# Performance work log

Measured on AMD Instinct MI355X. Metric: run time of the kernel, lower is better.

## Reference

```python
import jax, jax.numpy as jnp
import numpy as np

B, N1, N2, D = 4, 8192, 8192, 3

def setup_inputs() -> dict:
    key = jax.random.key(0)
    k1, k2 = jax.random.split(key)
    xyz1 = jax.random.normal(k1, (B, N1, D), dtype=jnp.float32)
    xyz2 = jax.random.normal(k2, (B, N2, D), dtype=jnp.float32)
    return {"xyz1": xyz1, "xyz2": xyz2}

def reference(xyz1, xyz2):
    # Pairwise squared distances via ||a-b||^2 = ||a||^2 + ||b||^2 - 2 a.b
    sq1 = jnp.sum(xyz1 * xyz1, axis=-1)                     # [B, N1]
    sq2 = jnp.sum(xyz2 * xyz2, axis=-1)                     # [B, N2]
    cross = jnp.einsum("bnd,bmd->bnm", xyz1, xyz2)          # [B, N1, N2]
    d = sq1[:, :, None] + sq2[:, None, :] - 2.0 * cross     # [B, N1, N2]
    dist1 = jnp.min(d, axis=2)                              # nearest in xyz2 for each xyz1 point
    dist2 = jnp.min(d, axis=1)                              # nearest in xyz1 for each xyz2 point
    return jnp.mean(dist1) + jnp.mean(dist2)                # reduction='mean'
```

## Files before the change

kernel.cpp:

```cpp
#include <hip/hip_runtime.h>
#include <math.h>

#define BATCH 4
#define NPTS  8192
#define TOTAL (BATCH * NPTS)
#define TPB   256

#define CT     2
#define WPB    (TPB / 64)
#define COLS_PER_WAVE  (32 * CT)
#define COLS_PER_BLOCK (COLS_PER_WAVE * WPB)
#define ROWCH  16
#define SWEEP  (NPTS / ROWCH)
#define NT     (SWEEP / 32)

typedef __bf16 bf16v8 __attribute__((ext_vector_type(8)));
typedef float  f32x16 __attribute__((ext_vector_type(16)));


__device__ __forceinline__ unsigned f2ord(float f) {
  unsigned b = __float_as_uint(f);
  return ((int)b >= 0) ? (b ^ 0x80000000u) : ~b;
}
__device__ __forceinline__ float ord2f(unsigned k) {
  unsigned b = (k & 0x80000000u) ? (k ^ 0x80000000u) : ~k;
  return __uint_as_float(b);
}
__device__ __forceinline__ unsigned short f2bf(float f) {
  unsigned u = __float_as_uint(f);
  return (unsigned short)((u + 0x7fffu + ((u >> 16) & 1u)) >> 16);
}
__device__ __forceinline__ float bf2f(unsigned short h) {
  return __uint_as_float(((unsigned)h) << 16);
}
__device__ __forceinline__ float mf3(float a, float b, float c) {
  return fminf(fminf(a, b), c);
}
__device__ __forceinline__ float coltree(const f32x16& a, float colt) {
  float t0 = mf3(a[0], a[1], a[2]);
  float t1 = mf3(a[3], a[4], a[5]);
  float t2 = mf3(a[6], a[7], a[8]);
  float t3 = mf3(a[9], a[10], a[11]);
  float t4 = mf3(a[12], a[13], a[14]);
  return mf3(colt, mf3(t0, t1, a[15]), mf3(t2, t3, t4));
}

__global__ __launch_bounds__(TPB) void pack_kernel(
    const float* __restrict__ x1, const float* __restrict__ x2,
    unsigned short* __restrict__ Af, unsigned short* __restrict__ Bf,
    unsigned* __restrict__ minbuf, float* __restrict__ out) {
  int i = blockIdx.x * TPB + threadIdx.x;
  if (i == 0) out[0] = 0.0f;
  minbuf[i] = 0xFFFFFFFFu;

  bool s2 = (i >= TOTAL);
  int j = s2 ? i - TOTAL : i;
  const float* src = s2 ? x2 : x1;
  float x = src[3 * j + 0];
  float y = src[3 * j + 1];
  float z = src[3 * j + 2];
  float sq = fmaf(x, x, fmaf(y, y, z * z));
  unsigned short sh = f2bf(sq);
  unsigned short sl = f2bf(sq - bf2f(sh));
  const unsigned short one = 0x3F80;

  unsigned short hx = f2bf(x), hy = f2bf(y), hz = f2bf(z);
  unsigned short lx = f2bf(x - bf2f(hx)), ly = f2bf(y - bf2f(hy)), lz = f2bf(z - bf2f(hz));
  float cx = -2.0f * x, cy = -2.0f * y, cz = -2.0f * z;
  unsigned short chx = f2bf(cx), chy = f2bf(cy), chz = f2bf(cz);
  unsigned short clx = f2bf(cx - bf2f(chx)), cly = f2bf(cy - bf2f(chy)), clz = f2bf(cz - bf2f(chz));

  {
    unsigned short v[16] = {hx, hy, hz, lx, ly, lz, hx, hy, hz,
                            sh, sl, one, one, 0, 0, 0};
    uint4* dst = (uint4*)(Af + (size_t)i * 16);
    uint4 w0, w1;
    w0.x = v[0] | ((unsigned)v[1] << 16);  w0.y = v[2] | ((unsigned)v[3] << 16);
    w0.z = v[4] | ((unsigned)v[5] << 16);  w0.w = v[6] | ((unsigned)v[7] << 16);
    w1.x = v[8] | ((unsigned)v[9] << 16);  w1.y = v[10] | ((unsigned)v[11] << 16);
    w1.z = v[12] | ((unsigned)v[13] << 16); w1.w = v[14] | ((unsigned)v[15] << 16);
    dst[0] = w0; dst[1] = w1;
  }
  {
    unsigned short v[16] = {chx, chy, chz, chx, chy, chz, clx, cly, clz,
                            one, one, sh, sl, 0, 0, 0};
    uint4* dst = (uint4*)(Bf + (size_t)i * 16);
    uint4 w0, w1;
    w0.x = v[0] | ((unsigned)v[1] << 16);  w0.y = v[2] | ((unsigned)v[3] << 16);
    w0.z = v[4] | ((unsigned)v[5] << 16);  w0.w = v[6] | ((unsigned)v[7] << 16);
    w1.x = v[8] | ((unsigned)v[9] << 16);  w1.y = v[10] | ((unsigned)v[11] << 16);
    w1.z = v[12] | ((unsigned)v[13] << 16); w1.w = v[14] | ((unsigned)v[15] << 16);
    dst[0] = w0; dst[1] = w1;
  }
}

__global__ __launch_bounds__(TPB, 6) void min_kernel(
    const unsigned short* __restrict__ Af, const unsigned short* __restrict__ Bf,
    unsigned* __restrict__ minbuf) {
  const int z   = blockIdx.z;
  const int b   = z & (BATCH - 1);
  const int dir = z >> 2;
  const int tid = threadIdx.x;
  const int wave = tid >> 6, lane = tid & 63;
  const int g = lane >> 5, l31 = lane & 31;

  const int colset = dir * TOTAL;
  const int rowset = TOTAL - colset;
  const int colbase = blockIdx.x * COLS_PER_BLOCK + wave * COLS_PER_WAVE;
  const int rowbase = blockIdx.y * SWEEP;

  const bf16v8* bv = (const bf16v8*)Bf;
  bf16v8 bfr0 = bv[(size_t)(colset + b * NPTS + colbase + l31) * 2 + g];
  bf16v8 bfr1 = bv[(size_t)(colset + b * NPTS + colbase + 32 + l31) * 2 + g];

  f32x16 zc;
#pragma unroll
  for (int q = 0; q < 16; ++q) zc[q] = 0.0f;
  float colacc0 = INFINITY, colacc1 = INFINITY;

  const bf16v8* ap = (const bf16v8*)Af + (size_t)(rowset + b * NPTS + rowbase + l31) * 2 + g;

  for (int ti = 0; ti < NT; ++ti) {
    bf16v8 a = ap[0];
    f32x16 acc0 = __builtin_amdgcn_mfma_f32_32x32x16_bf16(a, bfr0, zc, 0, 0, 0);
    f32x16 acc1 = __builtin_amdgcn_mfma_f32_32x32x16_bf16(a, bfr1, zc, 0, 0, 0);
    colacc0 = coltree(acc0, colacc0);
    colacc1 = coltree(acc1, colacc1);
    ap += 64;
  }

  {
    float m0 = fminf(colacc0, __shfl_xor(colacc0, 32));
    float m1 = fminf(colacc1, __shfl_xor(colacc1, 32));
    if (g == 0) {
      atomicMin(&minbuf[colset + b * NPTS + colbase + l31], f2ord(m0));
      atomicMin(&minbuf[colset + b * NPTS + colbase + 32 + l31], f2ord(m1));
    }
  }
}

__global__ __launch_bounds__(TPB) void finalize_kernel(
    const unsigned* __restrict__ minbuf, float* __restrict__ out, float scale) {
  int idx = blockIdx.x * TPB + threadIdx.x;
  float v = ord2f(minbuf[idx]) * scale;
  for (int off = 32; off > 0; off >>= 1) v += __shfl_down(v, off);
  __shared__ float ls[TPB / 64];
  if ((threadIdx.x & 63) == 0) ls[threadIdx.x >> 6] = v;
  __syncthreads();
  if (threadIdx.x == 0) {
    float t = 0.0f;
#pragma unroll
    for (int w = 0; w < TPB / 64; ++w) t += ls[w];
    atomicAdd(out, t);
  }
}

extern "C" void kernel_launch(void* const* d_in, const int* in_sizes, int n_in,
                              void* d_out, int out_size, void* d_ws, size_t ws_size,
                              hipStream_t stream) {
  const float* xyz1 = (const float*)d_in[0];
  const float* xyz2 = (const float*)d_in[1];
  float* out = (float*)d_out;

  char* ws = (char*)d_ws;
  unsigned short* Af = (unsigned short*)(ws);
  unsigned short* Bf = (unsigned short*)(ws + (size_t)2 * TOTAL * 32);
  unsigned*   minbuf = (unsigned*)(ws + (size_t)4 * TOTAL * 32);

  pack_kernel<<<dim3(2 * TOTAL / TPB), dim3(TPB), 0, stream>>>(
      xyz1, xyz2, Af, Bf, minbuf, out);

  dim3 mgrid(NPTS / COLS_PER_BLOCK, ROWCH, 2 * BATCH);
  min_kernel<<<mgrid, dim3(TPB), 0, stream>>>(Af, Bf, minbuf);

  const float scale = 1.0f / (float)TOTAL;
  finalize_kernel<<<dim3(2 * TOTAL / TPB), dim3(TPB), 0, stream>>>(minbuf, out, scale);
}
```

Measured before the change: 32.42 us.

## Compute each distance tile once and reduce both row and column minima

Result: slower. 99.49 us (+206.9%).

```diff
diff --git a/kernel.cpp b/kernel.cpp
--- a/kernel.cpp
+++ b/kernel.cpp
@@ -6,12 +6,10 @@
 #define TOTAL (BATCH * NPTS)
 #define TPB   256
 
-#define CT     2
-#define WPB    (TPB / 64)
-#define COLS_PER_WAVE  (32 * CT)
-#define COLS_PER_BLOCK (COLS_PER_WAVE * WPB)
-#define ROWCH  16
-#define SWEEP  (NPTS / ROWCH)
+#define WPB    4
+#define ROWS_PER_BLOCK (32 * WPB)
+#define COLCH  8
+#define SWEEP  (NPTS / COLCH)
 #define NT     (SWEEP / 32)
 
 typedef __bf16 bf16v8 __attribute__((ext_vector_type(8)));
@@ -33,17 +31,6 @@
 __device__ __forceinline__ float bf2f(unsigned short h) {
   return __uint_as_float(((unsigned)h) << 16);
 }
-__device__ __forceinline__ float mf3(float a, float b, float c) {
-  return fminf(fminf(a, b), c);
-}
-__device__ __forceinline__ float coltree(const f32x16& a, float colt) {
-  float t0 = mf3(a[0], a[1], a[2]);
-  float t1 = mf3(a[3], a[4], a[5]);
-  float t2 = mf3(a[6], a[7], a[8]);
-  float t3 = mf3(a[9], a[10], a[11]);
-  float t4 = mf3(a[12], a[13], a[14]);
-  return mf3(colt, mf3(t0, t1, a[15]), mf3(t2, t3, t4));
-}
 
 __global__ __launch_bounds__(TPB) void pack_kernel(
     const float* __restrict__ x1, const float* __restrict__ x2,
@@ -52,25 +39,16 @@
   int i = blockIdx.x * TPB + threadIdx.x;
   if (i == 0) out[0] = 0.0f;
   minbuf[i] = 0xFFFFFFFFu;
-
-  bool s2 = (i >= TOTAL);
-  int j = s2 ? i - TOTAL : i;
-  const float* src = s2 ? x2 : x1;
-  float x = src[3 * j + 0];
-  float y = src[3 * j + 1];
-  float z = src[3 * j + 2];
-  float sq = fmaf(x, x, fmaf(y, y, z * z));
-  unsigned short sh = f2bf(sq);
-  unsigned short sl = f2bf(sq - bf2f(sh));
+  minbuf[TOTAL + i] = 0xFFFFFFFFu;
   const unsigned short one = 0x3F80;
 
-  unsigned short hx = f2bf(x), hy = f2bf(y), hz = f2bf(z);
-  unsigned short lx = f2bf(x - bf2f(hx)), ly = f2bf(y - bf2f(hy)), lz = f2bf(z - bf2f(hz));
-  float cx = -2.0f * x, cy = -2.0f * y, cz = -2.0f * z;
-  unsigned short chx = f2bf(cx), chy = f2bf(cy), chz = f2bf(cz);
-  unsigned short clx = f2bf(cx - bf2f(chx)), cly = f2bf(cy - bf2f(chy)), clz = f2bf(cz - bf2f(chz));
-
   {
+    float x = x1[3 * i + 0], y = x1[3 * i + 1], z = x1[3 * i + 2];
+    float sq = fmaf(x, x, fmaf(y, y, z * z));
+    unsigned short sh = f2bf(sq);
+    unsigned short sl = f2bf(sq - bf2f(sh));
+    unsigned short hx = f2bf(x), hy = f2bf(y), hz = f2bf(z);
+    unsigned short lx = f2bf(x - bf2f(hx)), ly = f2bf(y - bf2f(hy)), lz = f2bf(z - bf2f(hz));
     unsigned short v[16] = {hx, hy, hz, lx, ly, lz, hx, hy, hz,
                             sh, sl, one, one, 0, 0, 0};
     uint4* dst = (uint4*)(Af + (size_t)i * 16);
@@ -82,6 +60,13 @@
     dst[0] = w0; dst[1] = w1;
   }
   {
+    float x = x2[3 * i + 0], y = x2[3 * i + 1], z = x2[3 * i + 2];
+    float sq = fmaf(x, x, fmaf(y, y, z * z));
+    unsigned short sh = f2bf(sq);
+    unsigned short sl = f2bf(sq - bf2f(sh));
+    float cx = -2.0f * x, cy = -2.0f * y, cz = -2.0f * z;
+    unsigned short chx = f2bf(cx), chy = f2bf(cy), chz = f2bf(cz);
+    unsigned short clx = f2bf(cx - bf2f(chx)), cly = f2bf(cy - bf2f(chy)), clz = f2bf(cz - bf2f(chz));
     unsigned short v[16] = {chx, chy, chz, chx, chy, chz, clx, cly, clz,
                             one, one, sh, sl, 0, 0, 0};
     uint4* dst = (uint4*)(Bf + (size_t)i * 16);
@@ -97,44 +82,60 @@
 __global__ __launch_bounds__(TPB, 6) void min_kernel(
     const unsigned short* __restrict__ Af, const unsigned short* __restrict__ Bf,
     unsigned* __restrict__ minbuf) {
-  const int z   = blockIdx.z;
-  const int b   = z & (BATCH - 1);
-  const int dir = z >> 2;
+  const int b   = blockIdx.z;
   const int tid = threadIdx.x;
   const int wave = tid >> 6, lane = tid & 63;
   const int g = lane >> 5, l31 = lane & 31;
 
-  const int colset = dir * TOTAL;
-  const int rowset = TOTAL - colset;
-  const int colbase = blockIdx.x * COLS_PER_BLOCK + wave * COLS_PER_WAVE;
-  const int rowbase = blockIdx.y * SWEEP;
+  const int rowbase = blockIdx.x * ROWS_PER_BLOCK + wave * 32;
+  const int colbase = blockIdx.y * SWEEP;
 
-  const bf16v8* bv = (const bf16v8*)Bf;
-  bf16v8 bfr0 = bv[(size_t)(colset + b * NPTS + colbase + l31) * 2 + g];
-  bf16v8 bfr1 = bv[(size_t)(colset + b * NPTS + colbase + 32 + l31) * 2 + g];
+  const bf16v8 af = *((const bf16v8*)Af + (size_t)(b * NPTS + rowbase + l31) * 2 + g);
 
   f32x16 zc;
 #pragma unroll
   for (int q = 0; q < 16; ++q) zc[q] = 0.0f;
-  float colacc0 = INFINITY, colacc1 = INFINITY;
 
-  const bf16v8* ap = (const bf16v8*)Af + (size_t)(rowset + b * NPTS + rowbase + l31) * 2 + g;
+  float rowacc[16];
+#pragma unroll
+  for (int q = 0; q < 16; ++q) rowacc[q] = INFINITY;
 
+  unsigned* __restrict__ d2 = minbuf + TOTAL + b * NPTS + colbase;
+  const bf16v8* bp = (const bf16v8*)Bf + (size_t)(b * NPTS + colbase + l31) * 2 + g;
+
+  bf16v8 bcur = bp[0];
   for (int ti = 0; ti < NT; ++ti) {
-    bf16v8 a = ap[0];
-    f32x16 acc0 = __builtin_amdgcn_mfma_f32_32x32x16_bf16(a, bfr0, zc, 0, 0, 0);
-    f32x16 acc1 = __builtin_amdgcn_mfma_f32_32x32x16_bf16(a, bfr1, zc, 0, 0, 0);
-    colacc0 = coltree(acc0, colacc0);
-    colacc1 = coltree(acc1, colacc1);
-    ap += 64;
+    bf16v8 bnext = bp[64];
+    f32x16 acc = __builtin_amdgcn_mfma_f32_32x32x16_bf16(af, bcur, zc, 0, 0, 0);
+
+#pragma unroll
+    for (int q = 0; q < 16; ++q) rowacc[q] = fminf(rowacc[q], acc[q]);
+
+    float ce = acc[0], co = acc[1];
+#pragma unroll
+    for (int k = 1; k < 8; ++k) {
+      ce = fminf(ce, acc[2 * k]);
+      co = fminf(co, acc[2 * k + 1]);
+    }
+    float m = fminf(ce, co);
+    m = fminf(m, __shfl_xor(m, 32));
+    if (g == 0) atomicMin(&d2[ti * 32 + l31], f2ord(m));
+
+    bcur = bnext;
+    bp += 64;
   }
 
-  {
-    float m0 = fminf(colacc0, __shfl_xor(colacc0, 32));
-    float m1 = fminf(colacc1, __shfl_xor(colacc1, 32));
-    if (g == 0) {
-      atomicMin(&minbuf[colset + b * NPTS + colbase + l31], f2ord(m0));
-      atomicMin(&minbuf[colset + b * NPTS + colbase + 32 + l31], f2ord(m1));
+#pragma unroll
+  for (int q = 0; q < 16; ++q) {
+    float v = rowacc[q];
+    v = fminf(v, __shfl_xor(v, 16));
+    v = fminf(v, __shfl_xor(v, 8));
+    v = fminf(v, __shfl_xor(v, 4));
+    v = fminf(v, __shfl_xor(v, 2));
+    v = fminf(v, __shfl_xor(v, 1));
+    if (l31 == 0) {
+      int row = rowbase + (q & 3) + 8 * (q >> 2) + 4 * g;
+      atomicMin(&minbuf[b * NPTS + row], f2ord(v));
     }
   }
 }
@@ -164,13 +165,13 @@
 
   char* ws = (char*)d_ws;
   unsigned short* Af = (unsigned short*)(ws);
-  unsigned short* Bf = (unsigned short*)(ws + (size_t)2 * TOTAL * 32);
-  unsigned*   minbuf = (unsigned*)(ws + (size_t)4 * TOTAL * 32);
+  unsigned short* Bf = (unsigned short*)(ws + (size_t)TOTAL * 32);
+  unsigned*   minbuf = (unsigned*)(ws + (size_t)2 * TOTAL * 32);
 
-  pack_kernel<<<dim3(2 * TOTAL / TPB), dim3(TPB), 0, stream>>>(
+  pack_kernel<<<dim3(TOTAL / TPB), dim3(TPB), 0, stream>>>(
       xyz1, xyz2, Af, Bf, minbuf, out);
 
-  dim3 mgrid(NPTS / COLS_PER_BLOCK, ROWCH, 2 * BATCH);
+  dim3 mgrid(NPTS / ROWS_PER_BLOCK, COLCH, BATCH);
   min_kernel<<<mgrid, dim3(TPB), 0, stream>>>(Af, Bf, minbuf);
 
   const float scale = 1.0f / (float)TOTAL;
```
